# Optimization experiments

Hardware: AMD Instinct MI355X
Metric: run time of the kernel (lower is better)

Reference implementation:

```python
import jax, jax.numpy as jnp
import numpy as np

BN_EPS = 1e-5
ATT_EPS = 1e-6


def _conv(x, w, groups=1):
    # x: [B,C,H,W], w: [O, C//groups, k, k], stride 1, SAME padding for odd k
    k = w.shape[-1]
    p = (k - 1) // 2
    return jax.lax.conv_general_dilated(
        x, w, window_strides=(1, 1), padding=[(p, p), (p, p)],
        dimension_numbers=('NCHW', 'OIHW', 'NCHW'), feature_group_count=groups)


def _bn(x, bnp):
    # bnp: [4, C] stacked (scale, bias, running_mean, running_var); eval-mode BN
    s, b, m, v = bnp[0], bnp[1], bnp[2], bnp[3]
    inv = s / jnp.sqrt(v + BN_EPS)
    return x * inv[None, :, None, None] + (b - m * inv)[None, :, None, None]


def _relu6(x):
    return jnp.clip(x, 0.0, 6.0)


def _ffn(x, fc1_w, fc1_bn, conv1_w, conv1_bn, conv2_w, conv2_bn, fc2_w, fc2_bn):
    # E_FFN: 1x1 ConvBNReLU6 -> dw5x5 ConvBNReLU6 & dw3x3 ConvBNReLU6 -> sum -> 1x1 ConvBN -> ReLU6
    C = x.shape[1]
    h = _relu6(_bn(_conv(x, fc1_w), fc1_bn))
    x1 = _relu6(_bn(_conv(h, conv1_w, groups=C), conv1_bn))
    x2 = _relu6(_bn(_conv(h, conv2_w, groups=C), conv2_bn))
    return _relu6(_bn(_conv(x1 + x2, fc2_w), fc2_bn))


def _bias(y, b):
    return y + b[None, :, None, None]


def setup_inputs() -> dict:
    key = jax.random.key(0)
    ks = jax.random.split(key, 16)
    C, M = 64, 8  # in_places, in_places // scale
    B, H, W = 4, 224, 224

    def w(k, shape, s=0.05):
        return (jax.random.normal(k, shape, dtype=jnp.float32) * s)

    def bn_params(k, c):
        k1, k2, k3, k4 = jax.random.split(k, 4)
        scale = 1.0 + 0.1 * jax.random.normal(k1, (c,), dtype=jnp.float32)
        bias = 0.1 * jax.random.normal(k2, (c,), dtype=jnp.float32)
        mean = 0.1 * jax.random.normal(k3, (c,), dtype=jnp.float32)
        var = 1.0 + 0.1 * jax.random.uniform(k4, (c,), dtype=jnp.float32)
        return jnp.stack([scale, bias, mean, var])  # [4, c]

    return {
        'x': jax.random.normal(ks[0], (B, C, H, W), dtype=jnp.float32),
        'gamma': jnp.full((1,), 0.5, dtype=jnp.float32),  # nonzero so attention branch matters
        'q_w': w(ks[1], (M, C, 1, 1)), 'q_b': w(ks[2], (M,)),
        'k_w': w(ks[3], (M, C, 1, 1)), 'k_b': w(ks[4], (M,)),
        'v_w': w(ks[5], (C, C, 1, 1)), 'v_b': w(ks[6], (C,)),
        'fc1_w': w(ks[7], (C, C, 1, 1)), 'fc1_bn': bn_params(ks[8], C),
        'conv1_w': w(ks[9], (C, 1, 5, 5)), 'conv1_bn': bn_params(ks[10], C),
        'conv2_w': w(ks[11], (C, 1, 3, 3)), 'conv2_bn': bn_params(ks[12], C),
        'fc2_w': w(ks[13], (C, C, 1, 1)), 'fc2_bn': bn_params(ks[14], C),
    }


def reference(x, gamma, q_w, q_b, k_w, k_b, v_w, v_b,
              fc1_w, fc1_bn, conv1_w, conv1_bn, conv2_w, conv2_bn, fc2_w, fc2_bn):
    B, C, H, W = x.shape
    N = H * W
    x_channel = _ffn(x, fc1_w, fc1_bn, conv1_w, conv1_bn, conv2_w, conv2_bn, fc2_w, fc2_bn)
    # softplus feature maps; Q,K: [B, m, N]
    Q = jax.nn.softplus(_bias(_conv(x, q_w), q_b).reshape(B, -1, N))
    K = jax.nn.softplus(_bias(_conv(x, k_w), k_b).reshape(B, -1, N))
    V = (_bias(_conv(x, v_w), v_b) + x_channel).reshape(B, C, N)
    Qt = jnp.swapaxes(Q, 1, 2)                              # [B, N, m]
    KV = jnp.einsum('bmn,bcn->bmc', K, V)                   # [B, m, C]
    norm = 1.0 / jnp.einsum('bnm,bm->bn', Qt, K.sum(-1) + ATT_EPS)  # [B, N]
    wv = jnp.einsum('bnm,bmc,bn->bcn', Qt, KV, norm).reshape(B, C, H, W)
    return x + gamma * wv
```

## Files before the change

kernel.cpp:

```cpp
#include <hip/hip_runtime.h>
#include <math.h>

#define B_ 4
#define C_ 64
#define M_ 8
#define H_ 224
#define W_ 224
#define N_ (H_*W_)
#define CN_ (C_*N_)
#define MN_ (M_*N_)
#define BCN_ (B_*CN_)
#define BMN_ (B_*MN_)

__device__ __forceinline__ float relu6f(float v){ return fminf(fmaxf(v,0.0f),6.0f); }
__device__ __forceinline__ float softplusf(float v){
  return v > 0.0f ? v + log1pf(expf(-v)) : log1pf(expf(v));
}

#define FMA4(A, W, X) { A.x = fmaf((W), (X).x, A.x); A.y = fmaf((W), (X).y, A.y); \
                        A.z = fmaf((W), (X).z, A.z); A.w = fmaf((W), (X).w, A.w); }

__global__ __launch_bounds__(256) void k_fc1k(const float* __restrict__ x,
                                              const float* __restrict__ w,
                                              const float* __restrict__ bn,
                                              const float* __restrict__ kw,
                                              const float* __restrict__ kb,
                                              float* __restrict__ h,
                                              float* __restrict__ Kq)
{
  __shared__ float xsl[2*1024];
  __shared__ float wl [2*512];
  __shared__ float kt [512];
  const int tid  = threadIdx.x;
  const int b    = blockIdx.x / 392;
  const int pg   = blockIdx.x % 392;
  const int pix0 = pg*128;
  const float* xb = x + (size_t)b*CN_ + pix0;

  for (int idx = tid; idx < 512; idx += 256) {
    const int c = idx >> 3, m = idx & 7;
    kt[idx] = kw[m*64 + c];
  }

  const int scp = tid >> 5;
  const int spx = (tid & 31) << 2;
  const int e0 = tid*2, e1 = tid*2+1;
  const int wc0 = e0 >> 6, wo0 = e0 & 63;
  const int wc1 = e1 >> 6, wo1 = e1 & 63;

  {
    const float4 xr = *(const float4*)(xb + (size_t)scp*N_ + spx);
    const float w0r = w[wo0*64 + wc0];
    const float w1r = w[wo1*64 + wc1];
    *(float4*)&xsl[scp*128 + spx] = xr;
    wl[e0] = w0r; wl[e1] = w1r;
  }
  __syncthreads();

  const int lane = tid & 63, wv_ = tid >> 6;
  const int och  = 2*wv_ + (lane >> 5);
  const int ocb  = och*8;
  const int px4  = (lane & 31) << 2;

  float4 ah[8];
  float4 ak = {0,0,0,0};
  #pragma unroll
  for (int i = 0; i < 8; ++i) ah[i] = make_float4(0.f,0.f,0.f,0.f);

  for (int ck = 0; ck < 8; ++ck) {
    const int cur = ck & 1, nxt = cur ^ 1;
    const float* xc = &xsl[cur*1024];
    const float* wc = &wl[cur*512];
    float4 xr; float w0r, w1r;
    if (ck < 7) {
      const int c0n = (ck+1)*8;
      xr  = *(const float4*)(xb + (size_t)(c0n + scp)*N_ + spx);
      w0r = w[wo0*64 + c0n + wc0];
      w1r = w[wo1*64 + c0n + wc1];
    }
    #pragma unroll
    for (int cp = 0; cp < 8; ++cp) {
      const float4 xv = *(const float4*)&xc[cp*128 + px4];
      const float4 w0 = *(const float4*)&wc[cp*64 + ocb];
      const float4 w1 = *(const float4*)&wc[cp*64 + ocb + 4];
      const float kvw = kt[(ck*8+cp)*8 + och];
      FMA4(ah[0], w0.x, xv); FMA4(ah[1], w0.y, xv);
      FMA4(ah[2], w0.z, xv); FMA4(ah[3], w0.w, xv);
      FMA4(ah[4], w1.x, xv); FMA4(ah[5], w1.y, xv);
      FMA4(ah[6], w1.z, xv); FMA4(ah[7], w1.w, xv);
      FMA4(ak, kvw, xv);
    }
    if (ck < 7) {
      *(float4*)&xsl[nxt*1024 + scp*128 + spx] = xr;
      wl[nxt*512 + e0] = w0r; wl[nxt*512 + e1] = w1r;
    }
    __syncthreads();
  }

  float* hb = h + (size_t)b*CN_ + pix0 + px4;
  #pragma unroll
  for (int o = 0; o < 8; ++o) {
    const int oc = ocb + o;
    const float inv  = bn[oc] / sqrtf(bn[192+oc] + 1e-5f);
    const float beta = bn[64+oc] - bn[128+oc]*inv;
    float4 o4;
    o4.x = relu6f(fmaf(ah[o].x, inv, beta));
    o4.y = relu6f(fmaf(ah[o].y, inv, beta));
    o4.z = relu6f(fmaf(ah[o].z, inv, beta));
    o4.w = relu6f(fmaf(ah[o].w, inv, beta));
    *(float4*)(hb + (size_t)oc*N_) = o4;
  }
  {
    const float kbm = kb[och];
    float4 q;
    q.x = softplusf(ak.x + kbm); q.y = softplusf(ak.y + kbm);
    q.z = softplusf(ak.z + kbm); q.w = softplusf(ak.w + kbm);
    *(float4*)(Kq + (size_t)b*MN_ + (size_t)och*N_ + pix0 + px4) = q;
  }
}

__global__ __launch_bounds__(256) void k_dw(const float* __restrict__ h,
                                            const float* __restrict__ w5,
                                            const float* __restrict__ w3,
                                            const float* __restrict__ bn1,
                                            const float* __restrict__ bn2,
                                            float* __restrict__ s)
{
  __shared__ float tile[36*37];
  const int tid = threadIdx.x;
  const int blk = blockIdx.x;
  const int t   = blk % 49;
  const int bc  = blk / 49;
  const int c   = bc & 63;
  const int tx0 = (t % 7) * 32;
  const int ty0 = (t / 7) * 32;
  const float* hb = h + (size_t)bc * N_;

  for (int idx = tid; idx < 1296; idx += 256) {
    const int ly = idx / 36, lx = idx - ly*36;
    const int gy = ty0 + ly - 2, gx = tx0 + lx - 2;
    float v = 0.0f;
    if (gy >= 0 && gy < H_ && gx >= 0 && gx < W_) v = hb[gy*W_ + gx];
    tile[ly*37 + lx] = v;
  }
  __syncthreads();

  float w5r[25], w3r[9];
  #pragma unroll
  for (int i = 0; i < 25; ++i) w5r[i] = w5[c*25 + i];
  #pragma unroll
  for (int i = 0; i < 9; ++i)  w3r[i] = w3[c*9 + i];
  const float inv1 = bn1[c] / sqrtf(bn1[192+c] + 1e-5f);
  const float bet1 = bn1[64+c] - bn1[128+c]*inv1;
  const float inv2 = bn2[c] / sqrtf(bn2[192+c] + 1e-5f);
  const float bet2 = bn2[64+c] - bn2[128+c]*inv2;

  const int ty  = tid >> 3;
  const int tx4 = (tid & 7) << 2;
  float a5[4] = {0,0,0,0}, a3[4] = {0,0,0,0};
  #pragma unroll
  for (int dy = 0; dy < 5; ++dy) {
    float r[8];
    #pragma unroll
    for (int i = 0; i < 8; ++i) r[i] = tile[(ty+dy)*37 + tx4 + i];
    #pragma unroll
    for (int dx = 0; dx < 5; ++dx) {
      const float wv = w5r[dy*5+dx];
      #pragma unroll
      for (int p = 0; p < 4; ++p) a5[p] = fmaf(wv, r[p+dx], a5[p]);
    }
    if (dy >= 1 && dy <= 3) {
      #pragma unroll
      for (int dx = 1; dx <= 3; ++dx) {
        const float wv = w3r[(dy-1)*3+(dx-1)];
        #pragma unroll
        for (int p = 0; p < 4; ++p) a3[p] = fmaf(wv, r[p+dx], a3[p]);
      }
    }
  }
  float* sb = s + (size_t)bc * N_ + (ty0+ty)*W_ + tx0 + tx4;
  float4 o4;
  o4.x = relu6f(fmaf(a5[0],inv1,bet1)) + relu6f(fmaf(a3[0],inv2,bet2));
  o4.y = relu6f(fmaf(a5[1],inv1,bet1)) + relu6f(fmaf(a3[1],inv2,bet2));
  o4.z = relu6f(fmaf(a5[2],inv1,bet1)) + relu6f(fmaf(a3[2],inv2,bet2));
  o4.w = relu6f(fmaf(a5[3],inv1,bet1)) + relu6f(fmaf(a3[3],inv2,bet2));
  *(float4*)sb = o4;
}

__global__ __launch_bounds__(256) void k_v(const float* __restrict__ x,
                                           const float* __restrict__ s,
                                           const float* __restrict__ vw,
                                           const float* __restrict__ vb,
                                           const float* __restrict__ fw,
                                           const float* __restrict__ fbn,
                                           float* __restrict__ V)
{
  __shared__ float xsl[2*1024];
  __shared__ float ssl[2*1024];
  __shared__ float wvl[2*512];
  __shared__ float wfl[2*512];
  const int tid  = threadIdx.x;
  const int b    = blockIdx.x / 392;
  const int pg   = blockIdx.x % 392;
  const int pix0 = pg*128;
  const float* xb = x + (size_t)b*CN_ + pix0;
  const float* sb = s + (size_t)b*CN_ + pix0;

  const int scp = tid >> 5;
  const int spx = (tid & 31) << 2;
  const int e0 = tid*2, e1 = tid*2+1;
  const int wc0 = e0 >> 6, wo0 = e0 & 63;
  const int wc1 = e1 >> 6, wo1 = e1 & 63;

  {
    const float4 xr = *(const float4*)(xb + (size_t)scp*N_ + spx);
    const float4 sr = *(const float4*)(sb + (size_t)scp*N_ + spx);
    const float a0 = vw[wo0*64 + wc0], a1 = vw[wo1*64 + wc1];
    const float f0 = fw[wo0*64 + wc0], f1 = fw[wo1*64 + wc1];
    *(float4*)&xsl[scp*128 + spx] = xr;
    *(float4*)&ssl[scp*128 + spx] = sr;
    wvl[e0] = a0; wvl[e1] = a1;
    wfl[e0] = f0; wfl[e1] = f1;
  }
  __syncthreads();

  const int lane = tid & 63, wv_ = tid >> 6;
  const int och  = 2*wv_ + (lane >> 5);
  const int ocb  = och*8;
  const int px4  = (lane & 31) << 2;

  float4 av[8], af[8];
  #pragma unroll
  for (int i = 0; i < 8; ++i) { av[i] = make_float4(0,0,0,0); af[i] = make_float4(0,0,0,0); }

  for (int ck = 0; ck < 8; ++ck) {
    const int cur = ck & 1, nxt = cur ^ 1;
    const float* xc = &xsl[cur*1024];
    const float* sc2 = &ssl[cur*1024];
    const float* wvc = &wvl[cur*512];
    const float* wfc = &wfl[cur*512];
    float4 xr, sr; float a0r, a1r, f0r, f1r;
    if (ck < 7) {
      const int c0n = (ck+1)*8;
      xr  = *(const float4*)(xb + (size_t)(c0n + scp)*N_ + spx);
      sr  = *(const float4*)(sb + (size_t)(c0n + scp)*N_ + spx);
      a0r = vw[wo0*64 + c0n + wc0]; a1r = vw[wo1*64 + c0n + wc1];
      f0r = fw[wo0*64 + c0n + wc0]; f1r = fw[wo1*64 + c0n + wc1];
    }
    #pragma unroll
    for (int cp = 0; cp < 8; ++cp) {
      const float4 xv = *(const float4*)&xc[cp*128 + px4];
      const float4 sv = *(const float4*)&sc2[cp*128 + px4];
      const float4 wa0 = *(const float4*)&wvc[cp*64 + ocb];
      const float4 wa1 = *(const float4*)&wvc[cp*64 + ocb + 4];
      const float4 wf0 = *(const float4*)&wfc[cp*64 + ocb];
      const float4 wf1 = *(const float4*)&wfc[cp*64 + ocb + 4];
      FMA4(av[0], wa0.x, xv); FMA4(av[1], wa0.y, xv);
      FMA4(av[2], wa0.z, xv); FMA4(av[3], wa0.w, xv);
      FMA4(av[4], wa1.x, xv); FMA4(av[5], wa1.y, xv);
      FMA4(av[6], wa1.z, xv); FMA4(av[7], wa1.w, xv);
      FMA4(af[0], wf0.x, sv); FMA4(af[1], wf0.y, sv);
      FMA4(af[2], wf0.z, sv); FMA4(af[3], wf0.w, sv);
      FMA4(af[4], wf1.x, sv); FMA4(af[5], wf1.y, sv);
      FMA4(af[6], wf1.z, sv); FMA4(af[7], wf1.w, sv);
    }
    if (ck < 7) {
      *(float4*)&xsl[nxt*1024 + scp*128 + spx] = xr;
      *(float4*)&ssl[nxt*1024 + scp*128 + spx] = sr;
      wvl[nxt*512 + e0] = a0r; wvl[nxt*512 + e1] = a1r;
      wfl[nxt*512 + e0] = f0r; wfl[nxt*512 + e1] = f1r;
    }
    __syncthreads();
  }

  float* Vb = V + (size_t)b*CN_ + pix0 + px4;
  #pragma unroll
  for (int o = 0; o < 8; ++o) {
    const int oc = ocb + o;
    const float inv  = fbn[oc] / sqrtf(fbn[192+oc] + 1e-5f);
    const float beta = fbn[64+oc] - fbn[128+oc]*inv;
    const float bias = vb[oc];
    float4 o4;
    o4.x = av[o].x + bias + relu6f(fmaf(af[o].x, inv, beta));
    o4.y = av[o].y + bias + relu6f(fmaf(af[o].y, inv, beta));
    o4.z = av[o].z + bias + relu6f(fmaf(af[o].z, inv, beta));
    o4.w = av[o].w + bias + relu6f(fmaf(af[o].w, inv, beta));
    *(float4*)(Vb + (size_t)oc*N_) = o4;
  }
}

__global__ __launch_bounds__(256) void k_kv(const float* __restrict__ V,
                                            const float* __restrict__ Kq,
                                            float* __restrict__ KV,
                                            float* __restrict__ Ksum)
{
  const int blk = blockIdx.x;
  const int b   = blk >> 7;
  const int rem = blk & 127;
  const int cg  = rem >> 4;
  const int ch  = rem & 15;
  const int tid = threadIdx.x;
  const int base = ch * 3136;
  const int end  = base + 3136;
  const float* Kb = Kq + (size_t)b*MN_;
  const float* Vb = V  + (size_t)b*CN_ + (size_t)(cg*8)*N_;

  float acc[64];
  #pragma unroll
  for (int i = 0; i < 64; ++i) acc[i] = 0.0f;
  float ks[8] = {0,0,0,0,0,0,0,0};

  for (int n = base + tid; n < end; n += 256) {
    float kv[8];
    #pragma unroll
    for (int m2 = 0; m2 < 8; ++m2) kv[m2] = Kb[m2*N_ + n];
    #pragma unroll
    for (int m2 = 0; m2 < 8; ++m2) ks[m2] += kv[m2];
    #pragma unroll
    for (int c8 = 0; c8 < 8; ++c8) {
      const float vv = Vb[c8*N_ + n];
      #pragma unroll
      for (int m2 = 0; m2 < 8; ++m2)
        acc[m2*8+c8] = fmaf(kv[m2], vv, acc[m2*8+c8]);
    }
  }
  const int lane = tid & 63;
  float mine = 0.0f;
  #pragma unroll
  for (int jj = 0; jj < 64; ++jj) {
    float v = acc[jj];
    v += __shfl_xor(v, 1);
    v += __shfl_xor(v, 2);
    v += __shfl_xor(v, 4);
    v += __shfl_xor(v, 8);
    v += __shfl_xor(v, 16);
    v += __shfl_xor(v, 32);
    if (lane == jj) mine = v;
  }
  atomicAdd(&KV[b*512 + (lane>>3)*64 + cg*8 + (lane&7)], mine);
  if (cg == 0) {
    float mk = 0.0f;
    #pragma unroll
    for (int jj = 0; jj < 8; ++jj) {
      float v = ks[jj];
      v += __shfl_xor(v, 1);
      v += __shfl_xor(v, 2);
      v += __shfl_xor(v, 4);
      v += __shfl_xor(v, 8);
      v += __shfl_xor(v, 16);
      v += __shfl_xor(v, 32);
      if (lane == jj) mk = v;
    }
    if (lane < 8) atomicAdd(&Ksum[b*8 + lane], mk);
  }
}

__global__ __launch_bounds__(256) void k_out(const float* __restrict__ x,
                                             const float* __restrict__ qw,
                                             const float* __restrict__ qb,
                                             const float* __restrict__ gamma,
                                             const float* __restrict__ KV,
                                             const float* __restrict__ Ksum,
                                             float* __restrict__ out)
{
  __shared__ float xs[64*256];
  __shared__ __align__(16) float kvt[64*8];
  __shared__ __align__(16) float wqt[64*8];
  __shared__ float ksl[8];
  const int tid = threadIdx.x;
  const int b  = blockIdx.x / 196;
  const int pg = blockIdx.x % 196;
  const int pix0 = pg*256;
  const float* xb = x + (size_t)b*CN_ + pix0;

  for (int idx = tid; idx < 512; idx += 256) {
    const int m = idx >> 6, c = idx & 63;
    kvt[c*8 + m] = KV[b*512 + idx];
    wqt[c*8 + m] = qw[idx];
  }
  if (tid < 8) ksl[tid] = Ksum[b*8 + tid] + 1e-6f;
  for (int idx = tid; idx < 4096; idx += 256) {
    const int c = idx >> 6, i = idx & 63;
    const float4 v = ((const float4*)(xb + (size_t)c*N_))[i];
    ((float4*)&xs[c*256])[i] = v;
  }
  __syncthreads();

  float q[8] = {0,0,0,0,0,0,0,0};
  #pragma unroll 8
  for (int c = 0; c < 64; ++c) {
    const float xv = xs[c*256 + tid];
    const float4 w0 = *(const float4*)&wqt[c*8];
    const float4 w1 = *(const float4*)&wqt[c*8+4];
    q[0] = fmaf(w0.x, xv, q[0]);
    q[1] = fmaf(w0.y, xv, q[1]);
    q[2] = fmaf(w0.z, xv, q[2]);
    q[3] = fmaf(w0.w, xv, q[3]);
    q[4] = fmaf(w1.x, xv, q[4]);
    q[5] = fmaf(w1.y, xv, q[5]);
    q[6] = fmaf(w1.z, xv, q[6]);
    q[7] = fmaf(w1.w, xv, q[7]);
  }
  float den = 0.0f;
  #pragma unroll
  for (int m = 0; m < 8; ++m) {
    q[m] = softplusf(q[m] + qb[m]);
    den  = fmaf(q[m], ksl[m], den);
  }
  const float sc = gamma[0] / den;

  float* ob = out + (size_t)b*CN_ + pix0 + tid;
  #pragma unroll 8
  for (int c = 0; c < 64; ++c) {
    const float4 k0 = *(const float4*)&kvt[c*8];
    const float4 k1 = *(const float4*)&kvt[c*8+4];
    float wv;
    wv = q[0]*k0.x;
    wv = fmaf(q[1], k0.y, wv);
    wv = fmaf(q[2], k0.z, wv);
    wv = fmaf(q[3], k0.w, wv);
    wv = fmaf(q[4], k1.x, wv);
    wv = fmaf(q[5], k1.y, wv);
    wv = fmaf(q[6], k1.z, wv);
    wv = fmaf(q[7], k1.w, wv);
    ob[(size_t)c*N_] = fmaf(sc, wv, xs[c*256 + tid]);
  }
}

extern "C" void kernel_launch(void* const* d_in, const int* in_sizes, int n_in,
                              void* d_out, int out_size, void* d_ws, size_t ws_size,
                              hipStream_t stream) {
  const float* x      = (const float*)d_in[0];
  const float* gamma  = (const float*)d_in[1];
  const float* q_w    = (const float*)d_in[2];
  const float* q_b    = (const float*)d_in[3];
  const float* k_w    = (const float*)d_in[4];
  const float* k_b    = (const float*)d_in[5];
  const float* v_w    = (const float*)d_in[6];
  const float* v_b    = (const float*)d_in[7];
  const float* fc1_w  = (const float*)d_in[8];
  const float* fc1_bn = (const float*)d_in[9];
  const float* c1_w   = (const float*)d_in[10];
  const float* c1_bn  = (const float*)d_in[11];
  const float* c2_w   = (const float*)d_in[12];
  const float* c2_bn  = (const float*)d_in[13];
  const float* fc2_w  = (const float*)d_in[14];
  const float* fc2_bn = (const float*)d_in[15];
  float* outp = (float*)d_out;

  float* ws   = (float*)d_ws;
  float* bufA = ws;
  float* bufS = ws + (size_t)BCN_;
  float* bufK = ws + (size_t)2*BCN_;
  float* kv   = ws + (size_t)2*BCN_ + BMN_;
  float* ksum = kv + 2048;

  hipMemsetAsync(kv, 0, (2048 + 32)*sizeof(float), stream);

  k_fc1k<<<dim3(B_*392), dim3(256), 0, stream>>>(x, fc1_w, fc1_bn, k_w, k_b, bufA, bufK);
  k_dw  <<<dim3(B_*C_*49), dim3(256), 0, stream>>>(bufA, c1_w, c2_w, c1_bn, c2_bn, bufS);
  k_v   <<<dim3(B_*392), dim3(256), 0, stream>>>(x, bufS, v_w, v_b, fc2_w, fc2_bn, bufA);
  k_kv  <<<dim3(512), dim3(256), 0, stream>>>(bufA, bufK, kv, ksum);
  k_out <<<dim3(B_*196), dim3(256), 0, stream>>>(x, q_w, q_b, gamma, kv, ksum, outp);
}
```

Baseline: 308.6 us.

## Fuse KV reduction into V kernel, compute Ksum in fc1, pad intermediate strides

The standalone KV reduction kernel is removed. Each V block now transposes its V tile into shared memory and reduces it against the matching K tile, adding the result into KV with atomics, so V is never written to or re-read from global memory. Ksum moves into the fc1/K kernel as a wavefront shuffle reduction followed by atomics. Intermediate buffers get a padded per-channel stride (50240) to avoid cache-set aliasing, and the output kernel reads x straight from global memory instead of staging 64KB of shared memory, which should raise occupancy. In exchange there are many more atomic adds, and the extra shared-memory pass with two barriers lengthens the V kernel.

```diff
diff --git a/kernel.cpp b/kernel.cpp
--- a/kernel.cpp
+++ b/kernel.cpp
@@ -7,10 +7,10 @@
 #define H_ 224
 #define W_ 224
 #define N_ (H_*W_)
+#define NP_ 50240
 #define CN_ (C_*N_)
-#define MN_ (M_*N_)
-#define BCN_ (B_*CN_)
-#define BMN_ (B_*MN_)
+#define CNP_ (C_*NP_)
+#define MNP_ (M_*NP_)
 
 __device__ __forceinline__ float relu6f(float v){ return fminf(fmaxf(v,0.0f),6.0f); }
 __device__ __forceinline__ float softplusf(float v){
@@ -26,7 +26,8 @@
                                               const float* __restrict__ kw,
                                               const float* __restrict__ kb,
                                               float* __restrict__ h,
-                                              float* __restrict__ Kq)
+                                              float* __restrict__ Kq,
+                                              float* __restrict__ Ksum)
 {
   __shared__ float xsl[2*1024];
   __shared__ float wl [2*512];
@@ -41,7 +42,6 @@
     const int c = idx >> 3, m = idx & 7;
     kt[idx] = kw[m*64 + c];
   }
-
   const int scp = tid >> 5;
   const int spx = (tid & 31) << 2;
   const int e0 = tid*2, e1 = tid*2+1;
@@ -97,7 +97,7 @@
     __syncthreads();
   }
 
-  float* hb = h + (size_t)b*CN_ + pix0 + px4;
+  float* hb = h + (size_t)b*CNP_ + pix0 + px4;
   #pragma unroll
   for (int o = 0; o < 8; ++o) {
     const int oc = ocb + o;
@@ -108,14 +108,21 @@
     o4.y = relu6f(fmaf(ah[o].y, inv, beta));
     o4.z = relu6f(fmaf(ah[o].z, inv, beta));
     o4.w = relu6f(fmaf(ah[o].w, inv, beta));
-    *(float4*)(hb + (size_t)oc*N_) = o4;
+    *(float4*)(hb + (size_t)oc*NP_) = o4;
   }
   {
     const float kbm = kb[och];
     float4 q;
     q.x = softplusf(ak.x + kbm); q.y = softplusf(ak.y + kbm);
     q.z = softplusf(ak.z + kbm); q.w = softplusf(ak.w + kbm);
-    *(float4*)(Kq + (size_t)b*MN_ + (size_t)och*N_ + pix0 + px4) = q;
+    *(float4*)(Kq + ((size_t)b*M_ + och)*NP_ + pix0 + px4) = q;
+    float part = q.x + q.y + q.z + q.w;
+    part += __shfl_xor(part, 1);
+    part += __shfl_xor(part, 2);
+    part += __shfl_xor(part, 4);
+    part += __shfl_xor(part, 8);
+    part += __shfl_xor(part, 16);
+    if ((lane & 31) == 0) atomicAdd(&Ksum[b*8 + och], part);
   }
 }
 
@@ -134,7 +141,7 @@
   const int c   = bc & 63;
   const int tx0 = (t % 7) * 32;
   const int ty0 = (t / 7) * 32;
-  const float* hb = h + (size_t)bc * N_;
+  const float* hb = h + (size_t)bc * NP_;
 
   for (int idx = tid; idx < 1296; idx += 256) {
     const int ly = idx / 36, lx = idx - ly*36;
@@ -178,7 +185,7 @@
       }
     }
   }
-  float* sb = s + (size_t)bc * N_ + (ty0+ty)*W_ + tx0 + tx4;
+  float* sb = s + (size_t)bc * NP_ + (ty0+ty)*W_ + tx0 + tx4;
   float4 o4;
   o4.x = relu6f(fmaf(a5[0],inv1,bet1)) + relu6f(fmaf(a3[0],inv2,bet2));
   o4.y = relu6f(fmaf(a5[1],inv1,bet1)) + relu6f(fmaf(a3[1],inv2,bet2));
@@ -187,24 +194,33 @@
   *(float4*)sb = o4;
 }
 
-__global__ __launch_bounds__(256) void k_v(const float* __restrict__ x,
-                                           const float* __restrict__ s,
-                                           const float* __restrict__ vw,
-                                           const float* __restrict__ vb,
-                                           const float* __restrict__ fw,
-                                           const float* __restrict__ fbn,
-                                           float* __restrict__ V)
+__global__ __launch_bounds__(256) void k_vkv(const float* __restrict__ x,
+                                             const float* __restrict__ s,
+                                             const float* __restrict__ vw,
+                                             const float* __restrict__ vb,
+                                             const float* __restrict__ fw,
+                                             const float* __restrict__ fbn,
+                                             const float* __restrict__ Kq,
+                                             float* __restrict__ KV)
 {
   __shared__ float xsl[2*1024];
   __shared__ float ssl[2*1024];
   __shared__ float wvl[2*512];
   __shared__ float wfl[2*512];
+  __shared__ float kts[8*128];
+  __shared__ float vts[128*33];
   const int tid  = threadIdx.x;
   const int b    = blockIdx.x / 392;
   const int pg   = blockIdx.x % 392;
   const int pix0 = pg*128;
-  const float* xb = x + (size_t)b*CN_ + pix0;
-  const float* sb = s + (size_t)b*CN_ + pix0;
+  const float* xb = x + (size_t)b*CN_  + pix0;
+  const float* sb = s + (size_t)b*CNP_ + pix0;
+
+  {
+    const float* Kb = Kq + (size_t)b*MNP_ + pix0;
+    for (int idx = tid; idx < 1024; idx += 256)
+      kts[idx] = Kb[(size_t)(idx>>7)*NP_ + (idx&127)];
+  }
 
   const int scp = tid >> 5;
   const int spx = (tid & 31) << 2;
@@ -213,8 +229,8 @@
   const int wc1 = e1 >> 6, wo1 = e1 & 63;
 
   {
-    const float4 xr = *(const float4*)(xb + (size_t)scp*N_ + spx);
-    const float4 sr = *(const float4*)(sb + (size_t)scp*N_ + spx);
+    const float4 xr = *(const float4*)(xb + (size_t)scp*N_  + spx);
+    const float4 sr = *(const float4*)(sb + (size_t)scp*NP_ + spx);
     const float a0 = vw[wo0*64 + wc0], a1 = vw[wo1*64 + wc1];
     const float f0 = fw[wo0*64 + wc0], f1 = fw[wo1*64 + wc1];
     *(float4*)&xsl[scp*128 + spx] = xr;
@@ -235,15 +251,15 @@
 
   for (int ck = 0; ck < 8; ++ck) {
     const int cur = ck & 1, nxt = cur ^ 1;
-    const float* xc = &xsl[cur*1024];
+    const float* xc  = &xsl[cur*1024];
     const float* sc2 = &ssl[cur*1024];
     const float* wvc = &wvl[cur*512];
     const float* wfc = &wfl[cur*512];
     float4 xr, sr; float a0r, a1r, f0r, f1r;
     if (ck < 7) {
       const int c0n = (ck+1)*8;
-      xr  = *(const float4*)(xb + (size_t)(c0n + scp)*N_ + spx);
-      sr  = *(const float4*)(sb + (size_t)(c0n + scp)*N_ + spx);
+      xr  = *(const float4*)(xb + (size_t)(c0n + scp)*N_  + spx);
+      sr  = *(const float4*)(sb + (size_t)(c0n + scp)*NP_ + spx);
       a0r = vw[wo0*64 + c0n + wc0]; a1r = vw[wo1*64 + c0n + wc1];
       f0r = fw[wo0*64 + c0n + wc0]; f1r = fw[wo1*64 + c0n + wc1];
     }
@@ -273,85 +289,41 @@
     __syncthreads();
   }
 
-  float* Vb = V + (size_t)b*CN_ + pix0 + px4;
+  float4 vf[8];
   #pragma unroll
   for (int o = 0; o < 8; ++o) {
     const int oc = ocb + o;
     const float inv  = fbn[oc] / sqrtf(fbn[192+oc] + 1e-5f);
     const float beta = fbn[64+oc] - fbn[128+oc]*inv;
     const float bias = vb[oc];
-    float4 o4;
-    o4.x = av[o].x + bias + relu6f(fmaf(af[o].x, inv, beta));
-    o4.y = av[o].y + bias + relu6f(fmaf(af[o].y, inv, beta));
-    o4.z = av[o].z + bias + relu6f(fmaf(af[o].z, inv, beta));
-    o4.w = av[o].w + bias + relu6f(fmaf(af[o].w, inv, beta));
-    *(float4*)(Vb + (size_t)oc*N_) = o4;
-  }
-}
-
-__global__ __launch_bounds__(256) void k_kv(const float* __restrict__ V,
-                                            const float* __restrict__ Kq,
-                                            float* __restrict__ KV,
-                                            float* __restrict__ Ksum)
-{
-  const int blk = blockIdx.x;
-  const int b   = blk >> 7;
-  const int rem = blk & 127;
-  const int cg  = rem >> 4;
-  const int ch  = rem & 15;
-  const int tid = threadIdx.x;
-  const int base = ch * 3136;
-  const int end  = base + 3136;
-  const float* Kb = Kq + (size_t)b*MN_;
-  const float* Vb = V  + (size_t)b*CN_ + (size_t)(cg*8)*N_;
-
-  float acc[64];
-  #pragma unroll
-  for (int i = 0; i < 64; ++i) acc[i] = 0.0f;
-  float ks[8] = {0,0,0,0,0,0,0,0};
-
-  for (int n = base + tid; n < end; n += 256) {
-    float kv[8];
-    #pragma unroll
-    for (int m2 = 0; m2 < 8; ++m2) kv[m2] = Kb[m2*N_ + n];
-    #pragma unroll
-    for (int m2 = 0; m2 < 8; ++m2) ks[m2] += kv[m2];
-    #pragma unroll
-    for (int c8 = 0; c8 < 8; ++c8) {
-      const float vv = Vb[c8*N_ + n];
+    vf[o].x = av[o].x + bias + relu6f(fmaf(af[o].x, inv, beta));
+    vf[o].y = av[o].y + bias + relu6f(fmaf(af[o].y, inv, beta));
+    vf[o].z = av[o].z + bias + relu6f(fmaf(af[o].z, inv, beta));
+    vf[o].w = av[o].w + bias + relu6f(fmaf(af[o].w, inv, beta));
+  }
+
+  #pragma unroll
+  for (int ph = 0; ph < 2; ++ph) {
+    if ((och >> 2) == ph) {
+      const int rb = ocb - ph*32;
       #pragma unroll
-      for (int m2 = 0; m2 < 8; ++m2)
-        acc[m2*8+c8] = fmaf(kv[m2], vv, acc[m2*8+c8]);
-    }
-  }
-  const int lane = tid & 63;
-  float mine = 0.0f;
-  #pragma unroll
-  for (int jj = 0; jj < 64; ++jj) {
-    float v = acc[jj];
-    v += __shfl_xor(v, 1);
-    v += __shfl_xor(v, 2);
-    v += __shfl_xor(v, 4);
-    v += __shfl_xor(v, 8);
-    v += __shfl_xor(v, 16);
-    v += __shfl_xor(v, 32);
-    if (lane == jj) mine = v;
-  }
-  atomicAdd(&KV[b*512 + (lane>>3)*64 + cg*8 + (lane&7)], mine);
-  if (cg == 0) {
-    float mk = 0.0f;
-    #pragma unroll
-    for (int jj = 0; jj < 8; ++jj) {
-      float v = ks[jj];
-      v += __shfl_xor(v, 1);
-      v += __shfl_xor(v, 2);
-      v += __shfl_xor(v, 4);
-      v += __shfl_xor(v, 8);
-      v += __shfl_xor(v, 16);
-      v += __shfl_xor(v, 32);
-      if (lane == jj) mk = v;
-    }
-    if (lane < 8) atomicAdd(&Ksum[b*8 + lane], mk);
+      for (int o = 0; o < 8; ++o) {
+        vts[(px4+0)*33 + rb+o] = vf[o].x;
+        vts[(px4+1)*33 + rb+o] = vf[o].y;
+        vts[(px4+2)*33 + rb+o] = vf[o].z;
+        vts[(px4+3)*33 + rb+o] = vf[o].w;
+      }
+    }
+    __syncthreads();
+    {
+      const int m = tid >> 5, cA = tid & 31;
+      float acc = 0.0f;
+      #pragma unroll 4
+      for (int px = 0; px < 128; ++px)
+        acc = fmaf(kts[m*128 + px], vts[px*33 + cA], acc);
+      atomicAdd(&KV[b*512 + m*64 + ph*32 + cA], acc);
+    }
+    __syncthreads();
   }
 }
 
@@ -363,68 +335,82 @@
                                              const float* __restrict__ Ksum,
                                              float* __restrict__ out)
 {
-  __shared__ float xs[64*256];
   __shared__ __align__(16) float kvt[64*8];
   __shared__ __align__(16) float wqt[64*8];
   __shared__ float ksl[8];
   const int tid = threadIdx.x;
   const int b  = blockIdx.x / 196;
   const int pg = blockIdx.x % 196;
-  const int pix0 = pg*256;
-  const float* xb = x + (size_t)b*CN_ + pix0;
-
+  const int px = pg*256 + tid;
   for (int idx = tid; idx < 512; idx += 256) {
     const int m = idx >> 6, c = idx & 63;
     kvt[c*8 + m] = KV[b*512 + idx];
     wqt[c*8 + m] = qw[idx];
   }
   if (tid < 8) ksl[tid] = Ksum[b*8 + tid] + 1e-6f;
-  for (int idx = tid; idx < 4096; idx += 256) {
-    const int c = idx >> 6, i = idx & 63;
-    const float4 v = ((const float4*)(xb + (size_t)c*N_))[i];
-    ((float4*)&xs[c*256])[i] = v;
-  }
   __syncthreads();
 
-  float q[8] = {0,0,0,0,0,0,0,0};
-  #pragma unroll 8
-  for (int c = 0; c < 64; ++c) {
-    const float xv = xs[c*256 + tid];
-    const float4 w0 = *(const float4*)&wqt[c*8];
-    const float4 w1 = *(const float4*)&wqt[c*8+4];
-    q[0] = fmaf(w0.x, xv, q[0]);
-    q[1] = fmaf(w0.y, xv, q[1]);
-    q[2] = fmaf(w0.z, xv, q[2]);
-    q[3] = fmaf(w0.w, xv, q[3]);
-    q[4] = fmaf(w1.x, xv, q[4]);
-    q[5] = fmaf(w1.y, xv, q[5]);
-    q[6] = fmaf(w1.z, xv, q[6]);
-    q[7] = fmaf(w1.w, xv, q[7]);
-  }
-  float den = 0.0f;
-  #pragma unroll
-  for (int m = 0; m < 8; ++m) {
-    q[m] = softplusf(q[m] + qb[m]);
-    den  = fmaf(q[m], ksl[m], den);
-  }
+  const float* xb = x + (size_t)b*CN_ + px;
+  float q0=0,q1=0,q2=0,q3=0,q4=0,q5=0,q6=0,q7=0;
+
+#define QSTEP(XV, CC) { \
+    const float4 wA = *(const float4*)&wqt[(CC)*8]; \
+    const float4 wB = *(const float4*)&wqt[(CC)*8+4]; \
+    q0=fmaf(wA.x,(XV),q0); q1=fmaf(wA.y,(XV),q1); \
+    q2=fmaf(wA.z,(XV),q2); q3=fmaf(wA.w,(XV),q3); \
+    q4=fmaf(wB.x,(XV),q4); q5=fmaf(wB.y,(XV),q5); \
+    q6=fmaf(wB.z,(XV),q6); q7=fmaf(wB.w,(XV),q7); }
+
+  #pragma unroll
+  for (int g = 0; g < 8; ++g) {
+    const int c0 = g*8;
+    const float x0 = xb[(size_t)(c0+0)*N_];
+    const float x1 = xb[(size_t)(c0+1)*N_];
+    const float x2 = xb[(size_t)(c0+2)*N_];
+    const float x3 = xb[(size_t)(c0+3)*N_];
+    const float x4 = xb[(size_t)(c0+4)*N_];
+    const float x5 = xb[(size_t)(c0+5)*N_];
+    const float x6 = xb[(size_t)(c0+6)*N_];
+    const float x7 = xb[(size_t)(c0+7)*N_];
+    QSTEP(x0,c0+0); QSTEP(x1,c0+1); QSTEP(x2,c0+2); QSTEP(x3,c0+3);
+    QSTEP(x4,c0+4); QSTEP(x5,c0+5); QSTEP(x6,c0+6); QSTEP(x7,c0+7);
+  }
+#undef QSTEP
+
+  q0 = softplusf(q0 + qb[0]); q1 = softplusf(q1 + qb[1]);
+  q2 = softplusf(q2 + qb[2]); q3 = softplusf(q3 + qb[3]);
+  q4 = softplusf(q4 + qb[4]); q5 = softplusf(q5 + qb[5]);
+  q6 = softplusf(q6 + qb[6]); q7 = softplusf(q7 + qb[7]);
+  float den = q0*ksl[0];
+  den = fmaf(q1, ksl[1], den); den = fmaf(q2, ksl[2], den);
+  den = fmaf(q3, ksl[3], den); den = fmaf(q4, ksl[4], den);
+  den = fmaf(q5, ksl[5], den); den = fmaf(q6, ksl[6], den);
+  den = fmaf(q7, ksl[7], den);
   const float sc = gamma[0] / den;
 
-  float* ob = out + (size_t)b*CN_ + pix0 + tid;
-  #pragma unroll 8
-  for (int c = 0; c < 64; ++c) {
-    const float4 k0 = *(const float4*)&kvt[c*8];
-    const float4 k1 = *(const float4*)&kvt[c*8+4];
-    float wv;
-    wv = q[0]*k0.x;
-    wv = fmaf(q[1], k0.y, wv);
-    wv = fmaf(q[2], k0.z, wv);
-    wv = fmaf(q[3], k0.w, wv);
-    wv = fmaf(q[4], k1.x, wv);
-    wv = fmaf(q[5], k1.y, wv);
-    wv = fmaf(q[6], k1.z, wv);
-    wv = fmaf(q[7], k1.w, wv);
-    ob[(size_t)c*N_] = fmaf(sc, wv, xs[c*256 + tid]);
-  }
+  float* ob = out + (size_t)b*CN_ + px;
+#define OSTEP(XV, CC) { \
+    const float4 kA = *(const float4*)&kvt[(CC)*8]; \
+    const float4 kB = *(const float4*)&kvt[(CC)*8+4]; \
+    float wv = q0*kA.x; wv=fmaf(q1,kA.y,wv); wv=fmaf(q2,kA.z,wv); wv=fmaf(q3,kA.w,wv); \
+    wv=fmaf(q4,kB.x,wv); wv=fmaf(q5,kB.y,wv); wv=fmaf(q6,kB.z,wv); wv=fmaf(q7,kB.w,wv); \
+    ob[(size_t)(CC)*N_] = fmaf(sc, wv, (XV)); }
+
+  #pragma unroll
+  for (int g = 0; g < 8; ++g) {
+    const int c0 = g*8;
+    const float x0 = xb[(size_t)(c0+0)*N_];
+    const float x1 = xb[(size_t)(c0+1)*N_];
+    const float x2 = xb[(size_t)(c0+2)*N_];
+    const float x3 = xb[(size_t)(c0+3)*N_];
+    const float x4 = xb[(size_t)(c0+4)*N_];
+    const float x5 = xb[(size_t)(c0+5)*N_];
+    const float x6 = xb[(size_t)(c0+6)*N_];
+    const float x7 = xb[(size_t)(c0+7)*N_];
+    OSTEP(x0,c0+0); OSTEP(x1,c0+1); OSTEP(x2,c0+2); OSTEP(x3,c0+3);
+    OSTEP(x4,c0+4); OSTEP(x5,c0+5); OSTEP(x6,c0+6); OSTEP(x7,c0+7);
+  }
+#undef OSTEP
 }
 
 extern "C" void kernel_launch(void* const* d_in, const int* in_sizes, int n_in,
@@ -449,17 +435,18 @@
   float* outp = (float*)d_out;
 
   float* ws   = (float*)d_ws;
-  float* bufA = ws;
-  float* bufS = ws + (size_t)BCN_;
-  float* bufK = ws + (size_t)2*BCN_;
-  float* kv   = ws + (size_t)2*BCN_ + BMN_;
+  float* bufH = ws;
+  float* bufS = bufH + (size_t)B_*CNP_;
+  float* bufK = bufS + (size_t)B_*CNP_;
+  float* kv   = bufK + (size_t)B_*MNP_;
   float* ksum = kv + 2048;
 
   hipMemsetAsync(kv, 0, (2048 + 32)*sizeof(float), stream);
 
-  k_fc1k<<<dim3(B_*392), dim3(256), 0, stream>>>(x, fc1_w, fc1_bn, k_w, k_b, bufA, bufK);
-  k_dw  <<<dim3(B_*C_*49), dim3(256), 0, stream>>>(bufA, c1_w, c2_w, c1_bn, c2_bn, bufS);
-  k_v   <<<dim3(B_*392), dim3(256), 0, stream>>>(x, bufS, v_w, v_b, fc2_w, fc2_bn, bufA);
-  k_kv  <<<dim3(512), dim3(256), 0, stream>>>(bufA, bufK, kv, ksum);
+  k_fc1k<<<dim3(B_*392), dim3(256), 0, stream>>>(x, fc1_w, fc1_bn, k_w, k_b,
+                                                 bufH, bufK, ksum);
+  k_dw  <<<dim3(B_*C_*49), dim3(256), 0, stream>>>(bufH, c1_w, c2_w, c1_bn, c2_bn, bufS);
+  k_vkv <<<dim3(B_*392), dim3(256), 0, stream>>>(x, bufS, v_w, v_b, fc2_w, fc2_bn,
+                                                 bufK, kv);
   k_out <<<dim3(B_*196), dim3(256), 0, stream>>>(x, q_w, q_b, gamma, kv, ksum, outp);
 }
```

New measurement: 406.6 us. 1.32x slower.

## Pad intermediate channel stride, move K-sum into fc1 kernel, widen V kernel blocks

Applied to the files above, without the earlier changes.

Intermediate buffers (h, s, V, K) now use a padded per-channel stride of 50240 instead of 50176. The padding is meant to avoid channel-strided accesses landing on the same cache and memory channels. The K column-sum is now computed with wave shuffles and atomics in the fc1/K kernel instead of inside the KV reduction kernel. The V kernel now uses 512-thread blocks over 256 pixels, doubling shared-memory tiles per block. These changes add atomics in fc1k and may reduce occupancy in k_v.

```diff
diff --git a/kernel.cpp b/kernel.cpp
--- a/kernel.cpp
+++ b/kernel.cpp
@@ -7,10 +7,10 @@
 #define H_ 224
 #define W_ 224
 #define N_ (H_*W_)
+#define NP_ 50240
 #define CN_ (C_*N_)
-#define MN_ (M_*N_)
-#define BCN_ (B_*CN_)
-#define BMN_ (B_*MN_)
+#define CNP_ (C_*NP_)
+#define MNP_ (M_*NP_)
 
 __device__ __forceinline__ float relu6f(float v){ return fminf(fmaxf(v,0.0f),6.0f); }
 __device__ __forceinline__ float softplusf(float v){
@@ -26,7 +26,8 @@
                                               const float* __restrict__ kw,
                                               const float* __restrict__ kb,
                                               float* __restrict__ h,
-                                              float* __restrict__ Kq)
+                                              float* __restrict__ Kq,
+                                              float* __restrict__ Ksum)
 {
   __shared__ float xsl[2*1024];
   __shared__ float wl [2*512];
@@ -41,7 +42,6 @@
     const int c = idx >> 3, m = idx & 7;
     kt[idx] = kw[m*64 + c];
   }
-
   const int scp = tid >> 5;
   const int spx = (tid & 31) << 2;
   const int e0 = tid*2, e1 = tid*2+1;
@@ -97,7 +97,7 @@
     __syncthreads();
   }
 
-  float* hb = h + (size_t)b*CN_ + pix0 + px4;
+  float* hb = h + (size_t)b*CNP_ + pix0 + px4;
   #pragma unroll
   for (int o = 0; o < 8; ++o) {
     const int oc = ocb + o;
@@ -108,14 +108,21 @@
     o4.y = relu6f(fmaf(ah[o].y, inv, beta));
     o4.z = relu6f(fmaf(ah[o].z, inv, beta));
     o4.w = relu6f(fmaf(ah[o].w, inv, beta));
-    *(float4*)(hb + (size_t)oc*N_) = o4;
+    *(float4*)(hb + (size_t)oc*NP_) = o4;
   }
   {
     const float kbm = kb[och];
     float4 q;
     q.x = softplusf(ak.x + kbm); q.y = softplusf(ak.y + kbm);
     q.z = softplusf(ak.z + kbm); q.w = softplusf(ak.w + kbm);
-    *(float4*)(Kq + (size_t)b*MN_ + (size_t)och*N_ + pix0 + px4) = q;
+    *(float4*)(Kq + ((size_t)b*M_ + och)*NP_ + pix0 + px4) = q;
+    float part = q.x + q.y + q.z + q.w;
+    part += __shfl_xor(part, 1);
+    part += __shfl_xor(part, 2);
+    part += __shfl_xor(part, 4);
+    part += __shfl_xor(part, 8);
+    part += __shfl_xor(part, 16);
+    if ((lane & 31) == 0) atomicAdd(&Ksum[b*8 + och], part);
   }
 }
 
@@ -134,7 +141,7 @@
   const int c   = bc & 63;
   const int tx0 = (t % 7) * 32;
   const int ty0 = (t / 7) * 32;
-  const float* hb = h + (size_t)bc * N_;
+  const float* hb = h + (size_t)bc * NP_;
 
   for (int idx = tid; idx < 1296; idx += 256) {
     const int ly = idx / 36, lx = idx - ly*36;
@@ -178,7 +185,7 @@
       }
     }
   }
-  float* sb = s + (size_t)bc * N_ + (ty0+ty)*W_ + tx0 + tx4;
+  float* sb = s + (size_t)bc * NP_ + (ty0+ty)*W_ + tx0 + tx4;
   float4 o4;
   o4.x = relu6f(fmaf(a5[0],inv1,bet1)) + relu6f(fmaf(a3[0],inv2,bet2));
   o4.y = relu6f(fmaf(a5[1],inv1,bet1)) + relu6f(fmaf(a3[1],inv2,bet2));
@@ -187,7 +194,7 @@
   *(float4*)sb = o4;
 }
 
-__global__ __launch_bounds__(256) void k_v(const float* __restrict__ x,
+__global__ __launch_bounds__(512) void k_v(const float* __restrict__ x,
                                            const float* __restrict__ s,
                                            const float* __restrict__ vw,
                                            const float* __restrict__ vb,
@@ -195,39 +202,36 @@
                                            const float* __restrict__ fbn,
                                            float* __restrict__ V)
 {
-  __shared__ float xsl[2*1024];
-  __shared__ float ssl[2*1024];
+  __shared__ float xsl[2*2048];
+  __shared__ float ssl[2*2048];
   __shared__ float wvl[2*512];
   __shared__ float wfl[2*512];
   const int tid  = threadIdx.x;
-  const int b    = blockIdx.x / 392;
-  const int pg   = blockIdx.x % 392;
-  const int pix0 = pg*128;
-  const float* xb = x + (size_t)b*CN_ + pix0;
-  const float* sb = s + (size_t)b*CN_ + pix0;
-
-  const int scp = tid >> 5;
-  const int spx = (tid & 31) << 2;
-  const int e0 = tid*2, e1 = tid*2+1;
-  const int wc0 = e0 >> 6, wo0 = e0 & 63;
-  const int wc1 = e1 >> 6, wo1 = e1 & 63;
+  const int b    = blockIdx.x / 196;
+  const int pg   = blockIdx.x % 196;
+  const int pix0 = pg*256;
+  const float* xb = x + (size_t)b*CN_  + pix0;
+  const float* sb = s + (size_t)b*CNP_ + pix0;
+
+  const int scp = tid >> 6;
+  const int spx = (tid & 63) << 2;
+  const int wc  = tid >> 6;
+  const int wo  = tid & 63;
 
   {
-    const float4 xr = *(const float4*)(xb + (size_t)scp*N_ + spx);
-    const float4 sr = *(const float4*)(sb + (size_t)scp*N_ + spx);
-    const float a0 = vw[wo0*64 + wc0], a1 = vw[wo1*64 + wc1];
-    const float f0 = fw[wo0*64 + wc0], f1 = fw[wo1*64 + wc1];
-    *(float4*)&xsl[scp*128 + spx] = xr;
-    *(float4*)&ssl[scp*128 + spx] = sr;
-    wvl[e0] = a0; wvl[e1] = a1;
-    wfl[e0] = f0; wfl[e1] = f1;
+    const float4 xr = *(const float4*)(xb + (size_t)scp*N_  + spx);
+    const float4 sr = *(const float4*)(sb + (size_t)scp*NP_ + spx);
+    const float a0 = vw[wo*64 + wc];
+    const float f0 = fw[wo*64 + wc];
+    *(float4*)&xsl[scp*256 + spx] = xr;
+    *(float4*)&ssl[scp*256 + spx] = sr;
+    wvl[tid] = a0; wfl[tid] = f0;
   }
   __syncthreads();
 
-  const int lane = tid & 63, wv_ = tid >> 6;
-  const int och  = 2*wv_ + (lane >> 5);
-  const int ocb  = och*8;
-  const int px4  = (lane & 31) << 2;
+  const int och = tid >> 6;
+  const int ocb = och*8;
+  const int px4 = (tid & 63) << 2;
 
   float4 av[8], af[8];
   #pragma unroll
@@ -235,22 +239,22 @@
 
   for (int ck = 0; ck < 8; ++ck) {
     const int cur = ck & 1, nxt = cur ^ 1;
-    const float* xc = &xsl[cur*1024];
-    const float* sc2 = &ssl[cur*1024];
+    const float* xc  = &xsl[cur*2048];
+    const float* sc2 = &ssl[cur*2048];
     const float* wvc = &wvl[cur*512];
     const float* wfc = &wfl[cur*512];
-    float4 xr, sr; float a0r, a1r, f0r, f1r;
+    float4 xr, sr; float a0r, f0r;
     if (ck < 7) {
       const int c0n = (ck+1)*8;
-      xr  = *(const float4*)(xb + (size_t)(c0n + scp)*N_ + spx);
-      sr  = *(const float4*)(sb + (size_t)(c0n + scp)*N_ + spx);
-      a0r = vw[wo0*64 + c0n + wc0]; a1r = vw[wo1*64 + c0n + wc1];
-      f0r = fw[wo0*64 + c0n + wc0]; f1r = fw[wo1*64 + c0n + wc1];
+      xr  = *(const float4*)(xb + (size_t)(c0n + scp)*N_  + spx);
+      sr  = *(const float4*)(sb + (size_t)(c0n + scp)*NP_ + spx);
+      a0r = vw[wo*64 + c0n + wc];
+      f0r = fw[wo*64 + c0n + wc];
     }
     #pragma unroll
     for (int cp = 0; cp < 8; ++cp) {
-      const float4 xv = *(const float4*)&xc[cp*128 + px4];
-      const float4 sv = *(const float4*)&sc2[cp*128 + px4];
+      const float4 xv  = *(const float4*)&xc [cp*256 + px4];
+      const float4 sv  = *(const float4*)&sc2[cp*256 + px4];
       const float4 wa0 = *(const float4*)&wvc[cp*64 + ocb];
       const float4 wa1 = *(const float4*)&wvc[cp*64 + ocb + 4];
       const float4 wf0 = *(const float4*)&wfc[cp*64 + ocb];
@@ -265,15 +269,15 @@
       FMA4(af[6], wf1.z, sv); FMA4(af[7], wf1.w, sv);
     }
     if (ck < 7) {
-      *(float4*)&xsl[nxt*1024 + scp*128 + spx] = xr;
-      *(float4*)&ssl[nxt*1024 + scp*128 + spx] = sr;
-      wvl[nxt*512 + e0] = a0r; wvl[nxt*512 + e1] = a1r;
-      wfl[nxt*512 + e0] = f0r; wfl[nxt*512 + e1] = f1r;
+      *(float4*)&xsl[nxt*2048 + scp*256 + spx] = xr;
+      *(float4*)&ssl[nxt*2048 + scp*256 + spx] = sr;
+      wvl[nxt*512 + tid] = a0r;
+      wfl[nxt*512 + tid] = f0r;
     }
     __syncthreads();
   }
 
-  float* Vb = V + (size_t)b*CN_ + pix0 + px4;
+  float* Vb = V + (size_t)b*CNP_ + pix0 + px4;
   #pragma unroll
   for (int o = 0; o < 8; ++o) {
     const int oc = ocb + o;
@@ -285,14 +289,13 @@
     o4.y = av[o].y + bias + relu6f(fmaf(af[o].y, inv, beta));
     o4.z = av[o].z + bias + relu6f(fmaf(af[o].z, inv, beta));
     o4.w = av[o].w + bias + relu6f(fmaf(af[o].w, inv, beta));
-    *(float4*)(Vb + (size_t)oc*N_) = o4;
+    *(float4*)(Vb + (size_t)oc*NP_) = o4;
   }
 }
 
 __global__ __launch_bounds__(256) void k_kv(const float* __restrict__ V,
                                             const float* __restrict__ Kq,
-                                            float* __restrict__ KV,
-                                            float* __restrict__ Ksum)
+                                            float* __restrict__ KV)
 {
   const int blk = blockIdx.x;
   const int b   = blk >> 7;
@@ -302,23 +305,20 @@
   const int tid = threadIdx.x;
   const int base = ch * 3136;
   const int end  = base + 3136;
-  const float* Kb = Kq + (size_t)b*MN_;
-  const float* Vb = V  + (size_t)b*CN_ + (size_t)(cg*8)*N_;
+  const float* Kb = Kq + (size_t)b*MNP_;
+  const float* Vb = V  + (size_t)b*CNP_ + (size_t)(cg*8)*NP_;
 
   float acc[64];
   #pragma unroll
   for (int i = 0; i < 64; ++i) acc[i] = 0.0f;
-  float ks[8] = {0,0,0,0,0,0,0,0};
 
   for (int n = base + tid; n < end; n += 256) {
     float kv[8];
     #pragma unroll
-    for (int m2 = 0; m2 < 8; ++m2) kv[m2] = Kb[m2*N_ + n];
-    #pragma unroll
-    for (int m2 = 0; m2 < 8; ++m2) ks[m2] += kv[m2];
+    for (int m2 = 0; m2 < 8; ++m2) kv[m2] = Kb[(size_t)m2*NP_ + n];
     #pragma unroll
     for (int c8 = 0; c8 < 8; ++c8) {
-      const float vv = Vb[c8*N_ + n];
+      const float vv = Vb[(size_t)c8*NP_ + n];
       #pragma unroll
       for (int m2 = 0; m2 < 8; ++m2)
         acc[m2*8+c8] = fmaf(kv[m2], vv, acc[m2*8+c8]);
@@ -338,21 +338,6 @@
     if (lane == jj) mine = v;
   }
   atomicAdd(&KV[b*512 + (lane>>3)*64 + cg*8 + (lane&7)], mine);
-  if (cg == 0) {
-    float mk = 0.0f;
-    #pragma unroll
-    for (int jj = 0; jj < 8; ++jj) {
-      float v = ks[jj];
-      v += __shfl_xor(v, 1);
-      v += __shfl_xor(v, 2);
-      v += __shfl_xor(v, 4);
-      v += __shfl_xor(v, 8);
-      v += __shfl_xor(v, 16);
-      v += __shfl_xor(v, 32);
-      if (lane == jj) mk = v;
-    }
-    if (lane < 8) atomicAdd(&Ksum[b*8 + lane], mk);
-  }
 }
 
 __global__ __launch_bounds__(256) void k_out(const float* __restrict__ x,
@@ -449,17 +434,18 @@
   float* outp = (float*)d_out;
 
   float* ws   = (float*)d_ws;
-  float* bufA = ws;
-  float* bufS = ws + (size_t)BCN_;
-  float* bufK = ws + (size_t)2*BCN_;
-  float* kv   = ws + (size_t)2*BCN_ + BMN_;
+  float* bufH = ws;
+  float* bufS = bufH + (size_t)B_*CNP_;
+  float* bufK = bufS + (size_t)B_*CNP_;
+  float* kv   = bufK + (size_t)B_*MNP_;
   float* ksum = kv + 2048;
 
   hipMemsetAsync(kv, 0, (2048 + 32)*sizeof(float), stream);
 
-  k_fc1k<<<dim3(B_*392), dim3(256), 0, stream>>>(x, fc1_w, fc1_bn, k_w, k_b, bufA, bufK);
-  k_dw  <<<dim3(B_*C_*49), dim3(256), 0, stream>>>(bufA, c1_w, c2_w, c1_bn, c2_bn, bufS);
-  k_v   <<<dim3(B_*392), dim3(256), 0, stream>>>(x, bufS, v_w, v_b, fc2_w, fc2_bn, bufA);
-  k_kv  <<<dim3(512), dim3(256), 0, stream>>>(bufA, bufK, kv, ksum);
+  k_fc1k<<<dim3(B_*392), dim3(256), 0, stream>>>(x, fc1_w, fc1_bn, k_w, k_b,
+                                                 bufH, bufK, ksum);
+  k_dw  <<<dim3(B_*C_*49), dim3(256), 0, stream>>>(bufH, c1_w, c2_w, c1_bn, c2_bn, bufS);
+  k_v   <<<dim3(B_*196), dim3(512), 0, stream>>>(x, bufS, v_w, v_b, fc2_w, fc2_bn, bufH);
+  k_kv  <<<dim3(512), dim3(256), 0, stream>>>(bufH, bufK, kv);
   k_out <<<dim3(B_*196), dim3(256), 0, stream>>>(x, q_w, q_b, gamma, kv, ksum, outp);
 }
```

Measured after the change: 360.7 us. 1.17x slower.
